# Kernel optimization log

Hardware: AMD Instinct MI355X
Metric: run time of the kernel (lower is better)

Reference implementation:

```python
import jax, jax.numpy as jnp
import numpy as np

NEG_SLOPE = 0.1

def leaky(x):
    return jnp.where(x >= 0, x, NEG_SLOPE * x)

def setup_inputs() -> dict:
    key = jax.random.key(0)
    ks = jax.random.split(key, 8)
    B, N, K, C, CO = 8, 16384, 9, 64, 64
    xy_offset = jax.random.normal(ks[0], (B, 2, N, K), dtype=jnp.float32)
    knn_features = jax.random.normal(ks[1], (B, C, N, K), dtype=jnp.float32)
    # WeightNet(2, [9, 9]): two 1x1 conv layers 2->9->9, leaky_relu after each
    wn_w1 = jax.random.normal(ks[2], (9, 2), dtype=jnp.float32) * (1.0 / np.sqrt(2))
    wn_b1 = jnp.zeros((9,), dtype=jnp.float32)
    wn_w2 = jax.random.normal(ks[3], (9, 9), dtype=jnp.float32) * (1.0 / 3.0)
    wn_b2 = jnp.zeros((9,), dtype=jnp.float32)
    # Linear(9*(C+2) -> CO)
    fan_in = 9 * (C + 2)
    lin_w = jax.random.normal(ks[4], (CO, fan_in), dtype=jnp.float32) * (1.0 / np.sqrt(fan_in))
    lin_b = jnp.zeros((CO,), dtype=jnp.float32)
    return {"xy_offset": xy_offset, "knn_features": knn_features,
            "wn_w1": wn_w1, "wn_b1": wn_b1, "wn_w2": wn_w2, "wn_b2": wn_b2,
            "lin_w": lin_w, "lin_b": lin_b}

def reference(xy_offset, knn_features, wn_w1, wn_b1, wn_w2, wn_b2, lin_w, lin_b):
    B, _, N, K = xy_offset.shape
    # concat positional offsets with features: [B, C+2, N, K]
    knn = jnp.concatenate([xy_offset, knn_features], axis=1)
    knn_cl = knn.transpose(0, 2, 3, 1)                       # [B, N, K, C+2]
    # WeightNet: 1x1 convs over channel dim of xy_offset
    h = leaky(jnp.einsum('oc,bcnk->bonk', wn_w1, xy_offset) + wn_b1[None, :, None, None])
    w = leaky(jnp.einsum('oc,bcnk->bonk', wn_w2, h) + wn_b2[None, :, None, None])  # [B, 9, N, K]
    w = w.transpose(0, 2, 1, 3)                              # [B, N, 9, K]
    # per-point small matmul: [B, N, 9, K] @ [B, N, K, C+2] -> [B, N, 9, C+2]
    wf = jnp.einsum('bnok,bnkc->bnoc', w, knn_cl)
    wf = wf.reshape(B, N, -1)                                # [B, N, 9*(C+2)]
    wf = wf @ lin_w.T + lin_b                                # [B, N, CO]
    out = leaky(wf.transpose(0, 2, 1))                       # [B, CO, N], norm=Identity
    return out
```

## Files before the change

### kernel.cpp

```cpp
#include <hip/hip_runtime.h>
#include <hip/hip_bf16.h>

#define NB   8
#define NN   16384
#define NK   9
#define NCF  64
#define NCIN 66
#define NCO  64
#define JTOT (NCIN * NK)
#define KPAD 608
#define ROWE 610
#define ROWU (ROWE / 2)
#define MT   32

typedef __attribute__((ext_vector_type(8))) short frag8;
typedef __attribute__((ext_vector_type(4))) float frag4;

__device__ __forceinline__ float leakyf(float x) { return fmaxf(x, 0.1f * x); }

__device__ __forceinline__ unsigned short f2bf(float x) {
  __hip_bfloat16 h = __float2bfloat16(x);
  unsigned short us;
  __builtin_memcpy(&us, &h, 2);
  return us;
}

__global__ void prep_lb_kernel(const float* __restrict__ lin_w, unsigned short* __restrict__ lb) {
  int idx = blockIdx.x * 256 + threadIdx.x;
  if (idx >= NCO * KPAD) return;
  int co = idx / KPAD;
  int j  = idx - co * KPAD;
  float v = 0.f;
  if (j < JTOT) {
    int c = j / NK;
    int o = j - c * NK;
    v = lin_w[co * JTOT + o * NCIN + c];
  }
  lb[idx] = f2bf(v);
}

__global__ __launch_bounds__(256) void pointconv_kernel(
    const float* __restrict__ xy,
    const float* __restrict__ feat,
    const float* __restrict__ w1,
    const float* __restrict__ b1,
    const float* __restrict__ w2,
    const float* __restrict__ b2,
    const unsigned short* __restrict__ lb,
    const float* __restrict__ lin_b,
    float* __restrict__ out) {
  __shared__ unsigned int wfu[MT * ROWU];

  const int t  = threadIdx.x;
  const int p  = t & 31;
  const int g  = t >> 5;
  const int b  = blockIdx.x >> 9;
  const int n0 = (blockIdx.x & 511) << 5;
  const int n  = n0 + p;

  float wv[9][9];
  {
    float x0[9], x1[9];
    const float* x0p = xy + (((size_t)b * 2 + 0) * NN + n) * NK;
    const float* x1p = xy + (((size_t)b * 2 + 1) * NN + n) * NK;
#pragma unroll
    for (int k = 0; k < NK; ++k) { x0[k] = x0p[k]; x1[k] = x1p[k]; }
#pragma unroll
    for (int k = 0; k < NK; ++k) {
      float h[9];
#pragma unroll
      for (int o = 0; o < 9; ++o)
        h[o] = leakyf(w1[2 * o] * x0[k] + w1[2 * o + 1] * x1[k] + b1[o]);
#pragma unroll
      for (int o = 0; o < 9; ++o) {
        float s = b2[o];
#pragma unroll
        for (int o2 = 0; o2 < 9; ++o2) s += w2[o * 9 + o2] * h[o2];
        wv[o][k] = leakyf(s);
      }
    }
  }

  const int cbeg = g * 8;
  float f0[4][9], f1[4][9];

  auto ldc = [&](float (&dst)[9], int c) {
    const float* fp = (c < 2)
        ? xy   + (((size_t)b * 2   + c)       * NN + n) * NK
        : feat + (((size_t)b * NCF + (c - 2)) * NN + n) * NK;
#pragma unroll
    for (int k = 0; k < NK; ++k) dst[k] = fp[k];
  };

  auto comp4 = [&](float (&f)[4][9], int c0) {
    unsigned int wo[18];
#pragma unroll
    for (int m = 0; m < 18; ++m) wo[m] = 0;
#pragma unroll
    for (int cc = 0; cc < 4; ++cc) {
#pragma unroll
      for (int o = 0; o < 9; ++o) {
        float s = wv[o][0] * f[cc][0];
#pragma unroll
        for (int k = 1; k < NK; ++k) s += wv[o][k] * f[cc][k];
        int v = cc * 9 + o;
        wo[v >> 1] |= (unsigned int)f2bf(s) << (16 * (v & 1));
      }
    }
    unsigned int* dst = wfu + p * ROWU + ((c0 * 9) >> 1);
#pragma unroll
    for (int m = 0; m < 18; ++m) dst[m] = wo[m];
  };

  auto comp2 = [&](float (&f)[4][9], int c0) {
    unsigned int wo[9];
#pragma unroll
    for (int m = 0; m < 9; ++m) wo[m] = 0;
#pragma unroll
    for (int cc = 0; cc < 2; ++cc) {
#pragma unroll
      for (int o = 0; o < 9; ++o) {
        float s = wv[o][0] * f[cc][0];
#pragma unroll
        for (int k = 1; k < NK; ++k) s += wv[o][k] * f[cc][k];
        int v = cc * 9 + o;
        wo[v >> 1] |= (unsigned int)f2bf(s) << (16 * (v & 1));
      }
    }
    unsigned int* dst = wfu + p * ROWU + ((c0 * 9) >> 1);
#pragma unroll
    for (int m = 0; m < 9; ++m) dst[m] = wo[m];
  };

#pragma unroll
  for (int cc = 0; cc < 4; ++cc) ldc(f0[cc], cbeg + cc);
#pragma unroll
  for (int cc = 0; cc < 4; ++cc) ldc(f1[cc], cbeg + 4 + cc);
  comp4(f0, cbeg + 0);
  if (g == 7) { ldc(f0[0], 64); ldc(f0[1], 65); }
  comp4(f1, cbeg + 4);
  if (g == 7) {
    comp2(f0, 64);
    unsigned int* dst = wfu + p * ROWU + 297;
#pragma unroll
    for (int m = 0; m < 7; ++m) dst[m] = 0;
  }
  __syncthreads();

  const int lane = t & 63;
  const int wvw  = t >> 6;
  const int r    = wvw & 1;
  const int hh   = wvw >> 1;
  const int col  = lane & 15;
  const int q    = lane >> 4;

  frag4 acc[2];
#pragma unroll
  for (int ct = 0; ct < 2; ++ct) acc[ct] = frag4{0.f, 0.f, 0.f, 0.f};

  const int arow_u = (16 * r + col) * ROWU;

  for (int s = 0; s < KPAD / 32; ++s) {
    const int k0 = 32 * s;
    union { unsigned int u[4]; frag8 v; } ua;
    const int abase = arow_u + ((k0 + q * 8) >> 1);
    ua.u[0] = wfu[abase + 0];
    ua.u[1] = wfu[abase + 1];
    ua.u[2] = wfu[abase + 2];
    ua.u[3] = wfu[abase + 3];
#pragma unroll
    for (int ct = 0; ct < 2; ++ct) {
      const frag8* bp = (const frag8*)(lb + ((2 * hh + ct) * 16 + col) * KPAD + k0 + q * 8);
      acc[ct] = __builtin_amdgcn_mfma_f32_16x16x32_bf16(ua.v, *bp, acc[ct], 0, 0, 0);
    }
  }

  float* outbase = out + ((size_t)b * NCO) * NN;
  const int nrow = n0 + 16 * r + q * 4;
#pragma unroll
  for (int ct = 0; ct < 2; ++ct) {
    const int co = (2 * hh + ct) * 16 + col;
    const float bias = lin_b[co];
    float4 v;
    v.x = leakyf(acc[ct][0] + bias);
    v.y = leakyf(acc[ct][1] + bias);
    v.z = leakyf(acc[ct][2] + bias);
    v.w = leakyf(acc[ct][3] + bias);
    *(float4*)(outbase + (size_t)co * NN + nrow) = v;
  }
}

extern "C" void kernel_launch(void* const* d_in, const int* in_sizes, int n_in,
                              void* d_out, int out_size, void* d_ws, size_t ws_size,
                              hipStream_t stream) {
  const float* xy    = (const float*)d_in[0];
  const float* feat  = (const float*)d_in[1];
  const float* w1    = (const float*)d_in[2];
  const float* b1    = (const float*)d_in[3];
  const float* w2    = (const float*)d_in[4];
  const float* b2    = (const float*)d_in[5];
  const float* lw    = (const float*)d_in[6];
  const float* lbias = (const float*)d_in[7];
  float* out = (float*)d_out;
  unsigned short* lb = (unsigned short*)d_ws;

  prep_lb_kernel<<<(NCO * KPAD + 255) / 256, 256, 0, stream>>>(lw, lb);
  pointconv_kernel<<<NB * (NN / MT), 256, 0, stream>>>(
      xy, feat, w1, b1, w2, b2, lb, lbias, out);
}
```

Before: 513.6 us.

## Stage feature chunks into LDS via global_load_lds for coalesced loads

Replaces per-thread strided 9-float feature loads with coalesced 16-byte global_load_lds transfers of 8-channel chunks into a shared staging buffer, then each thread reads its 9 values from LDS. The aim is to cut uncoalesced global traffic and register pressure from holding 8 channels of features per thread. In exchange it adds many block-wide barriers per chunk, serializes load and compute since there is a single stage buffer, and switches the LDS writes to 16-bit stores that may raise bank conflicts.

```diff
diff --git a/kernel.cpp b/kernel.cpp
--- a/kernel.cpp
+++ b/kernel.cpp
@@ -12,6 +12,11 @@
 #define ROWE 610
 #define ROWU (ROWE / 2)
 #define MT   32
+#define CHC  8
+#define NCHUNK (NCF / CHC)
+#define ROWB (MT * NK * 4)
+#define TRC  (CHC * ROWB / 16)
+#define INSC (TRC / 64)
 
 typedef __attribute__((ext_vector_type(8))) short frag8;
 typedef __attribute__((ext_vector_type(4))) float frag4;
@@ -49,18 +54,39 @@
     const unsigned short* __restrict__ lb,
     const float* __restrict__ lin_b,
     float* __restrict__ out) {
-  __shared__ unsigned int wfu[MT * ROWU];
-
-  const int t  = threadIdx.x;
-  const int p  = t & 31;
-  const int g  = t >> 5;
-  const int b  = blockIdx.x >> 9;
-  const int n0 = (blockIdx.x & 511) << 5;
-  const int n  = n0 + p;
+  __shared__ unsigned short wfs[MT * ROWE];
+  __shared__ float stage[CHC * MT * NK];
+
+  const int t    = threadIdx.x;
+  const int p    = t & 31;
+  const int g    = t >> 5;
+  const int lane = t & 63;
+  const int wvid = t >> 6;
+  const int b    = blockIdx.x >> 9;
+  const int n0   = (blockIdx.x & 511) << 5;
+  const int n    = n0 + p;
+
+  auto stage_chunk = [&](int ch) {
+    const char* gb = (const char*)feat +
+        (((size_t)b * NCF + ch * CHC) * NN + (size_t)n0) * (NK * 4);
+    for (int i = wvid; i < INSC; i += 4) {
+      unsigned j   = i * 64 + lane;
+      unsigned cl  = j / 72u;
+      unsigned rem = j - cl * 72u;
+      const char* gp = gb + (size_t)cl * ((size_t)NN * NK * 4) + rem * 16;
+      const char* lp = (const char*)stage + i * 1024;
+      __builtin_amdgcn_global_load_lds(
+          (const __attribute__((address_space(1))) unsigned int*)gp,
+          (__attribute__((address_space(3))) unsigned int*)lp,
+          16, 0, 0);
+    }
+  };
+
+  stage_chunk(0);
 
   float wv[9][9];
+  float x0[9], x1[9];
   {
-    float x0[9], x1[9];
     const float* x0p = xy + (((size_t)b * 2 + 0) * NN + n) * NK;
     const float* x1p = xy + (((size_t)b * 2 + 1) * NN + n) * NK;
 #pragma unroll
@@ -81,76 +107,50 @@
     }
   }
 
-  const int cbeg = g * 8;
-  float f0[4][9], f1[4][9];
-
-  auto ldc = [&](float (&dst)[9], int c) {
-    const float* fp = (c < 2)
-        ? xy   + (((size_t)b * 2   + c)       * NN + n) * NK
-        : feat + (((size_t)b * NCF + (c - 2)) * NN + n) * NK;
-#pragma unroll
-    for (int k = 0; k < NK; ++k) dst[k] = fp[k];
-  };
-
-  auto comp4 = [&](float (&f)[4][9], int c0) {
-    unsigned int wo[18];
-#pragma unroll
-    for (int m = 0; m < 18; ++m) wo[m] = 0;
-#pragma unroll
-    for (int cc = 0; cc < 4; ++cc) {
+  if (g == 0) {
+#pragma unroll
+    for (int cc = 0; cc < 2; ++cc) {
 #pragma unroll
       for (int o = 0; o < 9; ++o) {
-        float s = wv[o][0] * f[cc][0];
-#pragma unroll
-        for (int k = 1; k < NK; ++k) s += wv[o][k] * f[cc][k];
-        int v = cc * 9 + o;
-        wo[v >> 1] |= (unsigned int)f2bf(s) << (16 * (v & 1));
+        float s = wv[o][0] * (cc ? x1[0] : x0[0]);
+#pragma unroll
+        for (int k = 1; k < NK; ++k) s += wv[o][k] * (cc ? x1[k] : x0[k]);
+        wfs[p * ROWE + cc * 9 + o] = f2bf(s);
       }
     }
-    unsigned int* dst = wfu + p * ROWU + ((c0 * 9) >> 1);
-#pragma unroll
-    for (int m = 0; m < 18; ++m) dst[m] = wo[m];
-  };
-
-  auto comp2 = [&](float (&f)[4][9], int c0) {
-    unsigned int wo[9];
-#pragma unroll
-    for (int m = 0; m < 9; ++m) wo[m] = 0;
-#pragma unroll
-    for (int cc = 0; cc < 2; ++cc) {
+  }
+  if (g == 1) {
+#pragma unroll
+    for (int m = 0; m < KPAD - JTOT; ++m) wfs[p * ROWE + JTOT + m] = 0;
+  }
+
+  for (int ch = 0; ch < NCHUNK; ++ch) {
+    __syncthreads();
+    {
+      const float* sp = stage + g * (MT * NK) + p * NK;
+      float f[9];
+#pragma unroll
+      for (int k = 0; k < NK; ++k) f[k] = sp[k];
+      const int c = 2 + ch * CHC + g;
+      unsigned short* wr = wfs + p * ROWE + c * 9;
 #pragma unroll
       for (int o = 0; o < 9; ++o) {
-        float s = wv[o][0] * f[cc][0];
-#pragma unroll
-        for (int k = 1; k < NK; ++k) s += wv[o][k] * f[cc][k];
-        int v = cc * 9 + o;
-        wo[v >> 1] |= (unsigned int)f2bf(s) << (16 * (v & 1));
+        float s = wv[o][0] * f[0];
+#pragma unroll
+        for (int k = 1; k < NK; ++k) s += wv[o][k] * f[k];
+        wr[o] = f2bf(s);
       }
     }
-    unsigned int* dst = wfu + p * ROWU + ((c0 * 9) >> 1);
-#pragma unroll
-    for (int m = 0; m < 9; ++m) dst[m] = wo[m];
-  };
-
-#pragma unroll
-  for (int cc = 0; cc < 4; ++cc) ldc(f0[cc], cbeg + cc);
-#pragma unroll
-  for (int cc = 0; cc < 4; ++cc) ldc(f1[cc], cbeg + 4 + cc);
-  comp4(f0, cbeg + 0);
-  if (g == 7) { ldc(f0[0], 64); ldc(f0[1], 65); }
-  comp4(f1, cbeg + 4);
-  if (g == 7) {
-    comp2(f0, 64);
-    unsigned int* dst = wfu + p * ROWU + 297;
-#pragma unroll
-    for (int m = 0; m < 7; ++m) dst[m] = 0;
+    if (ch + 1 < NCHUNK) {
+      __syncthreads();
+      stage_chunk(ch + 1);
+    }
   }
   __syncthreads();
 
-  const int lane = t & 63;
-  const int wvw  = t >> 6;
-  const int r    = wvw & 1;
-  const int hh   = wvw >> 1;
+  const unsigned int* wfu = (const unsigned int*)wfs;
+  const int r    = wvid & 1;
+  const int hh   = wvid >> 1;
   const int col  = lane & 15;
   const int q    = lane >> 4;
 
```

Result: faster. 474.8 us (-7.6%).
